# Optimization experiments

Hardware: AMD Instinct MI355X
Metric: run time of the kernel (lower is better)

## Reference

```python
import jax, jax.numpy as jnp
import numpy as np

B, C, DD, HH, WW = 1, 128, 16, 16, 16
D_STATE, D_CONV, EXPAND = 16, 4, 2
D_INNER = EXPAND * C
DT_RANK = (C + 15) // 16


def setup_inputs():
    key = jax.random.key(0)
    ks = jax.random.split(key, 10)
    def w(k, shape, s=0.02):
        return jax.random.normal(k, shape, dtype=jnp.float32) * s
    return {
        "x": jax.random.normal(ks[0], (B, C, DD, HH, WW), dtype=jnp.float32),
        "ln_w": jnp.ones((C,), jnp.float32),
        "ln_b": jnp.zeros((C,), jnp.float32),
        "mnorm_w": jnp.ones((C,), jnp.float32),
        "mnorm_b": jnp.zeros((C,), jnp.float32),
        "in_proj_w": w(ks[1], (2 * D_INNER, C)),
        "conv_w": w(ks[2], (D_INNER, D_CONV), 0.2),
        "conv_b": jnp.zeros((D_INNER,), jnp.float32),
        "x_proj_w": w(ks[3], (DT_RANK + 2 * D_STATE, D_INNER)),
        "dt_proj_w": w(ks[4], (D_INNER, DT_RANK), 0.1),
        "dt_proj_b": jnp.full((D_INNER,), float(np.log(np.expm1(0.01))), jnp.float32),
        "A_log": jnp.log(jnp.tile(jnp.arange(1, D_STATE + 1, dtype=jnp.float32), (D_INNER, 1))),
        "D_param": jnp.ones((D_INNER,), jnp.float32),
        "out_proj_w": w(ks[5], (C, D_INNER)),
        "proj_w": w(ks[6], (C, 3 * C)),
        "proj_b": jnp.zeros((C,), jnp.float32),
        "fc1_w": w(ks[7], (4 * C, C)),
        "fc1_b": jnp.zeros((4 * C,), jnp.float32),
        "fc2_w": w(ks[8], (C, 4 * C)),
        "fc2_b": jnp.zeros((C,), jnp.float32),
    }


def _ln_cf(x, w, b, eps=1e-6):
    # channels_first LayerNorm over axis 1 (matches custom LayerNorm)
    u = x.mean(1, keepdims=True)
    s = ((x - u) ** 2).mean(1, keepdims=True)
    xn = (x - u) * jax.lax.rsqrt(s + eps)
    return w[None, :, None, None, None] * xn + b[None, :, None, None, None]


def _ln_last(x, w, b, eps=1e-5):
    u = x.mean(-1, keepdims=True)
    s = ((x - u) ** 2).mean(-1, keepdims=True)
    return (x - u) * jax.lax.rsqrt(s + eps) * w + b


def _selective_scan(u, delta, A, Bm, Cm, Dv):
    # u, delta: (N,L,d); Bm,Cm: (N,L,n); A: (d,n); Dv: (d,)
    dA = jnp.exp(delta[..., None] * A)                               # (N,L,d,n)
    dBu = delta[..., None] * Bm[:, :, None, :] * u[..., None]         # (N,L,d,n)
    def step(h, inp):
        dA_t, dBu_t, C_t = inp
        h = dA_t * h + dBu_t
        y = jnp.einsum("bdn,bn->bd", h, C_t)
        return h, y
    h0 = jnp.zeros((u.shape[0], A.shape[0], A.shape[1]), u.dtype)
    _, ys = jax.lax.scan(step, h0, (dA.swapaxes(0, 1), dBu.swapaxes(0, 1), Cm.swapaxes(0, 1)))
    return ys.swapaxes(0, 1) + u * Dv


def _mamba(xin, in_proj_w, conv_w, conv_b, x_proj_w, dt_proj_w, dt_proj_b, A_log, D_param, out_proj_w):
    # xin: (N, L, C)
    N, L, _ = xin.shape
    xz = xin @ in_proj_w.T                                            # (N,L,2*d_inner)
    xr, z = jnp.split(xz, 2, axis=-1)
    # causal depthwise conv1d, kernel D_CONV, left-padded (mamba conv1d[..., :L])
    xp = jnp.pad(xr, ((0, 0), (D_CONV - 1, 0), (0, 0)))
    xc = sum(conv_w[:, k] * xp[:, k:k + L, :] for k in range(D_CONV)) + conv_b
    xc = jax.nn.silu(xc)
    x_dbl = xc @ x_proj_w.T                                           # (N,L,dt_rank+2n)
    dt = x_dbl[..., :DT_RANK]
    Bm = x_dbl[..., DT_RANK:DT_RANK + D_STATE]
    Cm = x_dbl[..., DT_RANK + D_STATE:]
    delta = jax.nn.softplus(dt @ dt_proj_w.T + dt_proj_b)
    A = -jnp.exp(A_log)
    y = _selective_scan(xc, delta, A, Bm, Cm, D_param)
    y = y * jax.nn.silu(z)
    return y @ out_proj_w.T


def _forward(x, ln_w, ln_b, mnorm_w, mnorm_b, in_proj_w, conv_w, conv_b, x_proj_w, dt_proj_w, dt_proj_b, A_log, D_param, out_proj_w, proj_w, proj_b, fc1_w, fc1_b, fc2_w, fc2_b):
    Bb, Cc, Dd, Hh, Ww = x.shape
    L = Dd * Hh * Ww
    x1 = _ln_cf(x, ln_w, ln_b)
    # three directional flattenings (d-, h-, w-major); cube => shapes identical
    xd = x1.reshape(Bb, Cc, L)
    xh = x1.transpose(0, 1, 3, 4, 2).reshape(Bb, Cc, L)
    xw = x1.transpose(0, 1, 4, 2, 3).reshape(Bb, Cc, L)
    seq = jnp.stack([xd, xh, xw], 0).reshape(3 * Bb, Cc, L).swapaxes(1, 2)  # (3B,L,C)
    seq = _ln_last(seq, mnorm_w, mnorm_b)
    y = _mamba(seq, in_proj_w, conv_w, conv_b, x_proj_w, dt_proj_w, dt_proj_b, A_log, D_param, out_proj_w)
    # reassemble per-direction volumes (no inverse permute, matching torch code) and concat on channels
    cat = y.swapaxes(1, 2).reshape(3, Bb, Cc, Dd, Hh, Ww).transpose(1, 0, 2, 3, 4, 5).reshape(Bb, 3 * Cc, Dd, Hh, Ww)
    out1 = jnp.einsum("bkdhw,ok->bodhw", cat, proj_w) + proj_b[None, :, None, None, None]
    out_res = x + out1
    h = _ln_cf(out_res, ln_w, ln_b)
    h = jnp.einsum("bcdhw,oc->bodhw", h, fc1_w) + fc1_b[None, :, None, None, None]
    h = jax.nn.gelu(h, approximate=False)
    h = jnp.einsum("bcdhw,oc->bodhw", h, fc2_w) + fc2_b[None, :, None, None, None]
    return h + out_res


def reference(x, ln_w, ln_b, mnorm_w, mnorm_b, in_proj_w, conv_w, conv_b, x_proj_w, dt_proj_w, dt_proj_b, A_log, D_param, out_proj_w, proj_w, proj_b, fc1_w, fc1_b, fc2_w, fc2_b):
    return _forward(x, ln_w, ln_b, mnorm_w, mnorm_b, in_proj_w, conv_w, conv_b, x_proj_w, dt_proj_w, dt_proj_b, A_log, D_param, out_proj_w, proj_w, proj_b, fc1_w, fc1_b, fc2_w, fc2_b)
```

## Files before the change

### kernel.cpp

```cpp
#include <hip/hip_runtime.h>
#include <hip/hip_bf16.h>
#include <math.h>

#define L 4096
#define C 128
#define DI 256
#define NST 16
#define NS 3
#define NCH 256
#define CT 16
#define R3 12288

typedef unsigned short u16;

__device__ __forceinline__ float siluf(float x){ return x / (1.f + __expf(-x)); }
__device__ __forceinline__ float geluf(float x){ return 0.5f*x*(1.f + erff(x*0.70710678118654752f)); }

__device__ __forceinline__ float b2f(u16 h){ return __uint_as_float(((unsigned)h)<<16); }
__device__ __forceinline__ u16 f2b(float f){
  unsigned u = __float_as_uint(f);
  return (u16)((u + 0x7FFFu + ((u>>16)&1u)) >> 16);
}
__device__ __forceinline__ float4 b4f(const u16* p){
  ushort4 v = *(const ushort4*)p;
  return make_float4(b2f(v.x), b2f(v.y), b2f(v.z), b2f(v.w));
}

__device__ __forceinline__ int permf(int s, int l){
  if(s==0) return l;
  if(s==1) return ((l&15)<<8) | ((l>>8)<<4) | ((l>>4)&15);
  return (((l>>4)&15)<<8) | ((l&15)<<4) | (l>>8);
}

__global__ void k_M(const float* __restrict__ opw, const float* __restrict__ pw,
                    float* __restrict__ Mw){
  int b = blockIdx.x;
  int o = b & 127, s = b >> 7;
  int d = threadIdx.x;
  float acc = 0.f;
  for(int c=0;c<C;c++) acc += opw[c*DI + d] * pw[o*384 + s*128 + c];
  Mw[(s*256+d)*128 + o] = acc;
}

__global__ void k_lngemm(const float* __restrict__ x, const float* __restrict__ lw,
                         const float* __restrict__ lb, const float* __restrict__ mw,
                         const float* __restrict__ mb, const float* __restrict__ ipw,
                         u16* __restrict__ Zb){
  __shared__ float As[128][68];
  __shared__ float Bs[64][132];
  int p0 = blockIdx.x*64, j0 = blockIdx.y*64;
  int tid = threadIdx.x;
  for(int q=0;q<8;q++){
    int f = q*1024 + tid*4; int cc = f>>6, p = f&63;
    float4 v = *(const float4*)&x[cc*L + p0 + p];
    *(float4*)&As[cc][p] = v;
  }
  for(int q=0;q<8;q++){
    int f = q*1024 + tid*4; int j = f>>7, k = f&127;
    float4 b = *(const float4*)&ipw[(j0+j)*C + k];
    *(float4*)&Bs[j][k] = b;
  }
  __syncthreads();
  {
    int p = tid>>2, kg = tid&3;
    float s=0.f, sq=0.f;
    #pragma unroll
    for(int i=0;i<32;i++){
      int k = kg*32 + ((i + kg*2)&31);
      float v = As[k][p]; s += v; sq += v*v;
    }
    s  += __shfl_xor(s,1);  s  += __shfl_xor(s,2);
    sq += __shfl_xor(sq,1); sq += __shfl_xor(sq,2);
    float m1 = s*(1.f/C);
    float r1 = rsqrtf(sq*(1.f/C) - m1*m1 + 1e-6f);
    float s2=0.f, sq2=0.f;
    #pragma unroll
    for(int i=0;i<32;i++){
      int k = kg*32 + ((i + kg*2)&31);
      float t = lw[k]*((As[k][p]-m1)*r1) + lb[k];
      s2 += t; sq2 += t*t;
    }
    s2  += __shfl_xor(s2,1);  s2  += __shfl_xor(s2,2);
    sq2 += __shfl_xor(sq2,1); sq2 += __shfl_xor(sq2,2);
    float m2 = s2*(1.f/C);
    float r2 = rsqrtf(sq2*(1.f/C) - m2*m2 + 1e-5f);
    #pragma unroll
    for(int i=0;i<32;i++){
      int k = kg*32 + ((i + kg*2)&31);
      float t = lw[k]*((As[k][p]-m1)*r1) + lb[k];
      As[k][p] = mw[k]*((t-m2)*r2) + mb[k];
    }
  }
  __syncthreads();
  int og = tid & 15, r4 = tid >> 4;
  float acc[4][4] = {};
  for(int k=0;k<128;k++){
    float4 av = *(const float4*)&As[k][r4*4];
    float a[4] = {av.x, av.y, av.z, av.w};
    float b[4];
    #pragma unroll
    for(int j=0;j<4;j++) b[j] = Bs[og+16*j][k];
    #pragma unroll
    for(int i=0;i<4;i++)
      #pragma unroll
      for(int j=0;j<4;j++) acc[i][j] += a[i]*b[j];
  }
  #pragma unroll
  for(int i=0;i<4;i++)
    #pragma unroll
    for(int j=0;j<4;j++)
      Zb[(p0+r4*4+i)*512 + j0 + og + 16*j] = f2b(acc[i][j]);
}

__global__ void k_conv(const u16* __restrict__ Zb, const float* __restrict__ cw,
                       const float* __restrict__ cb, u16* __restrict__ xcb){
  int bl = blockIdx.x;
  int s = bl >> 12, l = bl & 4095;
  int d = threadIdx.x;
  float acc = cb[d];
  #pragma unroll
  for(int k=0;k<4;k++){
    int lk = l - 3 + k;
    if(lk >= 0){
      int p = permf(s, lk);
      acc += cw[d*4+k] * b2f(Zb[p*512 + d]);
    }
  }
  xcb[bl*DI + d] = f2b(siluf(acc));
}

__global__ void k_xd4a(const u16* __restrict__ xcb, const float* __restrict__ xpw,
                       float* __restrict__ xp){
  __shared__ float As[32][132];
  __shared__ float Ws[40][132];
  int r0 = blockIdx.x*32;
  int k0 = blockIdx.y*128;
  int tid = threadIdx.x;
  for(int q=0;q<4;q++){
    int f = q*256 + tid; int r = f>>5, kk = (f&31)*4;
    float4 v = b4f(&xcb[(r0+r)*DI + k0 + kk]);
    *(float4*)&As[r][kk] = v;
  }
  for(int q=0;q<5;q++){
    int f = q*256 + tid; int col = f>>5, kk = (f&31)*4;
    float4 v = *(const float4*)&xpw[col*DI + k0 + kk];
    *(float4*)&Ws[col][kk] = v;
  }
  __syncthreads();
  int r = tid & 31, cg = tid >> 5;
  float acc[5] = {0.f,0.f,0.f,0.f,0.f};
  for(int k4=0;k4<32;k4++){
    float4 a = *(const float4*)&As[r][k4*4];
    #pragma unroll
    for(int j=0;j<5;j++){
      float4 w = *(const float4*)&Ws[cg*5+j][k4*4];
      acc[j] += a.x*w.x + a.y*w.y + a.z*w.z + a.w*w.w;
    }
  }
  float* dst = xp + (blockIdx.y*12288 + r0 + r)*40 + cg*5;
  #pragma unroll
  for(int j=0;j<5;j++) dst[j] = acc[j];
}

__global__ void k_xd4b(const float* __restrict__ xp, const float* __restrict__ dtw,
                       const float* __restrict__ dtb, float* __restrict__ Bc,
                       float* __restrict__ Cc, u16* __restrict__ deltab){
  __shared__ float xdb[40][17];
  int r0 = blockIdx.x*16;
  int tid = threadIdx.x;
  for(int e=tid; e<640; e+=256){
    int row = e/40, col = e%40;
    int idx = (r0+row)*40 + col;
    xdb[col][row] = xp[idx] + xp[491520 + idx];
  }
  __syncthreads();
  {
    float4 ww0 = *(const float4*)&dtw[tid*8];
    float4 ww1 = *(const float4*)&dtw[tid*8+4];
    float bb = dtb[tid];
    #pragma unroll 4
    for(int r=0;r<16;r++){
      float aa = bb + xdb[0][r]*ww0.x + xdb[1][r]*ww0.y + xdb[2][r]*ww0.z + xdb[3][r]*ww0.w
                    + xdb[4][r]*ww1.x + xdb[5][r]*ww1.y + xdb[6][r]*ww1.z + xdb[7][r]*ww1.w;
      float dl = (aa > 20.f) ? aa : log1pf(__expf(aa));
      deltab[(r0+r)*DI + tid] = f2b(dl);
    }
  }
  if(tid < 64){
    int rr = tid>>2, ng = (tid&3)*4;
    float4 bv = make_float4(xdb[8+ng][rr], xdb[9+ng][rr], xdb[10+ng][rr], xdb[11+ng][rr]);
    *(float4*)&Bc[(r0+rr)*NST + ng] = bv;
  } else if(tid < 128){
    int t2 = tid - 64;
    int rr = t2>>2, ng = (t2&3)*4;
    float4 cv = make_float4(xdb[24+ng][rr], xdb[25+ng][rr], xdb[26+ng][rr], xdb[27+ng][rr]);
    *(float4*)&Cc[(r0+rr)*NST + ng] = cv;
  }
}

__global__ void k_scanA(const u16* __restrict__ deltab, const u16* __restrict__ xcb,
                        const float* __restrict__ Bc, const float* __restrict__ A_log,
                        u16* __restrict__ aggAb, u16* __restrict__ aggBb){
  int b = blockIdx.x;
  int ng = b & 3, ch = (b>>2)&255, s = b>>10;
  int d = threadIdx.x;
  int n0 = ng*4;
  float Aa[4], P[4] = {1.f,1.f,1.f,1.f}, S[4] = {0.f,0.f,0.f,0.f};
  #pragma unroll
  for(int j=0;j<4;j++) Aa[j] = -__expf(A_log[d*NST + n0 + j]);
  int base = s*L + ch*CT;
  #pragma unroll
  for(int st=0; st<CT; st++){
    int row = base + st;
    float dl = b2f(deltab[row*DI + d]);
    float u  = b2f(xcb[row*DI + d]);
    float4 bv = *(const float4*)&Bc[row*NST + n0];
    float dlu = dl*u;
    float a;
    a = __expf(dl*Aa[0]); S[0] = a*S[0] + dlu*bv.x; P[0] *= a;
    a = __expf(dl*Aa[1]); S[1] = a*S[1] + dlu*bv.y; P[1] *= a;
    a = __expf(dl*Aa[2]); S[2] = a*S[2] + dlu*bv.z; P[2] *= a;
    a = __expf(dl*Aa[3]); S[3] = a*S[3] + dlu*bv.w; P[3] *= a;
  }
  int idx0 = ch*R3 + s*256 + d;
  #pragma unroll
  for(int j=0;j<4;j++){
    int idx = idx0 + (n0+j)*768;
    aggAb[idx] = f2b(P[j]); aggBb[idx] = f2b(S[j]);
  }
}

__global__ void k_scanB(const u16* __restrict__ aggAb, const u16* __restrict__ aggBb,
                        u16* __restrict__ hInb){
  __shared__ float PA[32][9], PB[32][9];
  int tid = threadIdx.x;
  int jl = tid & 31, seg = tid >> 5;
  int j = blockIdx.x*32 + jl;
  int c0 = seg*32;
  float pa[32], pb[32];
  float P = 1.f, S = 0.f;
  #pragma unroll
  for(int i=0;i<32;i++){
    pa[i] = P; pb[i] = S;
    float a = b2f(aggAb[(c0+i)*R3 + j]), b = b2f(aggBb[(c0+i)*R3 + j]);
    S = a*S + b; P = a*P;
  }
  PA[jl][seg] = P; PB[jl][seg] = S;
  __syncthreads();
  if(tid < 32){
    float h = 0.f;
    #pragma unroll
    for(int sg=0; sg<8; sg++){
      float p = PA[tid][sg], s2 = PB[tid][sg];
      PA[tid][sg] = h;
      h = p*h + s2;
    }
  }
  __syncthreads();
  float h0 = PA[jl][seg];
  #pragma unroll
  for(int i=0;i<32;i++){
    hInb[(c0+i)*R3 + j] = f2b(pa[i]*h0 + pb[i]);
  }
}

__global__ void k_scanC(const u16* __restrict__ deltab, const u16* __restrict__ xcb,
                        const float* __restrict__ Bc, const float* __restrict__ Cc,
                        const float* __restrict__ A_log, const float* __restrict__ Dp,
                        const u16* __restrict__ Zb, const u16* __restrict__ hInb,
                        u16* __restrict__ yzb){
  int b = blockIdx.x;
  int ch = b & 255, s = b >> 8;
  int d = threadIdx.x;
  float Aa[16], h[16];
  #pragma unroll
  for(int n=0;n<16;n++) Aa[n] = -__expf(A_log[d*NST + n]);
  #pragma unroll
  for(int n=0;n<16;n++) h[n] = b2f(hInb[ch*R3 + n*768 + s*256 + d]);
  float Dv = Dp[d];
  int base = s*L + ch*CT;
  #pragma unroll 2
  for(int st=0; st<CT; st++){
    int row = base + st;
    float dl = b2f(deltab[row*DI + d]);
    float u  = b2f(xcb[row*DI + d]);
    float dlu = dl*u;
    const float4* Bp = (const float4*)&Bc[row*NST];
    const float4* Cp = (const float4*)&Cc[row*NST];
    float y = u*Dv;
    #pragma unroll
    for(int q=0;q<4;q++){
      float4 bv = Bp[q], cv = Cp[q];
      float a;
      a = __expf(dl*Aa[4*q+0]); h[4*q+0] = a*h[4*q+0] + dlu*bv.x; y += h[4*q+0]*cv.x;
      a = __expf(dl*Aa[4*q+1]); h[4*q+1] = a*h[4*q+1] + dlu*bv.y; y += h[4*q+1]*cv.y;
      a = __expf(dl*Aa[4*q+2]); h[4*q+2] = a*h[4*q+2] + dlu*bv.z; y += h[4*q+2]*cv.z;
      a = __expf(dl*Aa[4*q+3]); h[4*q+3] = a*h[4*q+3] + dlu*bv.w; y += h[4*q+3]*cv.w;
    }
    int l = ch*CT + st;
    int p = permf(s, l);
    float zv = b2f(Zb[p*512 + 256 + d]);
    yzb[(s*L + l)*DI + d] = f2b(y * siluf(zv));
  }
}

__global__ void k_proj(const u16* __restrict__ yzb, const float* __restrict__ Mw,
                       u16* __restrict__ ppb){
  __shared__ float As[64][68];
  __shared__ float Bs[64][132];
  int p0 = blockIdx.x*64; int kc = blockIdx.y;
  int s = kc >> 1, d0 = (kc & 1)*128;
  int tid = threadIdx.x;
  int og = tid & 15, r4 = tid >> 4;
  float acc[4][8] = {};
  for(int kk=0; kk<2; kk++){
    int kb = d0 + kk*64;
    for(int q=0;q<4;q++){
      int f = q*256 + tid; int r = f>>4, k = (f&15)*4;
      float4 a = b4f(&yzb[(s*L + p0 + r)*DI + kb + k]);
      *(float4*)&As[r][k] = a;
    }
    for(int q=0;q<8;q++){
      int f = q*1024 + tid*4; int k = f>>7, o = f&127;
      float4 b = *(const float4*)&Mw[(s*256 + kb + k)*128 + o];
      *(float4*)&Bs[k][o] = b;
    }
    __syncthreads();
    for(int k=0;k<64;k++){
      float a[4];
      #pragma unroll
      for(int i=0;i<4;i++) a[i] = As[r4*4+i][k];
      #pragma unroll
      for(int j=0;j<8;j++){
        float bb = Bs[k][og+16*j];
        #pragma unroll
        for(int i=0;i<4;i++) acc[i][j] += a[i]*bb;
      }
    }
    __syncthreads();
  }
  u16* dst = ppb + kc*524288;
  #pragma unroll
  for(int i=0;i<4;i++)
    #pragma unroll
    for(int j=0;j<8;j++)
      dst[(p0+r4*4+i)*C + og + 16*j] = f2b(acc[i][j]);
}

__global__ void k_pred(const u16* __restrict__ ppb, const float* __restrict__ x,
                       const float* __restrict__ pb, float* __restrict__ ores){
  __shared__ float Xs[16][129];
  int p0 = blockIdx.x*16; int tid = threadIdx.x;
  for(int q=0;q<8;q++){
    int f = q*256 + tid; int pl = f&15, o = f>>4;
    Xs[pl][o] = x[o*L + p0 + pl];
  }
  __syncthreads();
  for(int q=0;q<8;q++){
    int f = q*256 + tid; int o = f&127, pl = f>>7;
    int idx = (p0+pl)*C + o;
    float v = b2f(ppb[idx]) + b2f(ppb[524288+idx]) + b2f(ppb[1048576+idx])
            + b2f(ppb[1572864+idx]) + b2f(ppb[2097152+idx]) + b2f(ppb[2621440+idx]);
    ores[idx] = v + Xs[pl][o] + pb[o];
  }
}

__global__ void k_fc1(const float* __restrict__ ores, const float* __restrict__ lw,
                      const float* __restrict__ lb, const float* __restrict__ w1,
                      const float* __restrict__ b1, u16* __restrict__ Hb){
  __shared__ float As[64][129];
  __shared__ float Bs[64][129];
  int p0 = blockIdx.x*64, j0 = blockIdx.y*64;
  int tid = threadIdx.x;
  for(int q=0;q<8;q++){
    int f = q*1024 + tid*4; int r = f>>7, k = f&127;
    float4 a = *(const float4*)&ores[(p0+r)*C + k];
    As[r][k]=a.x; As[r][k+1]=a.y; As[r][k+2]=a.z; As[r][k+3]=a.w;
    float4 b = *(const float4*)&w1[(j0+r)*C + k];
    Bs[r][k]=b.x; Bs[r][k+1]=b.y; Bs[r][k+2]=b.z; Bs[r][k+3]=b.w;
  }
  __syncthreads();
  {
    int r = tid>>2, kg = tid&3;
    float s=0.f, sq=0.f;
    #pragma unroll
    for(int i=0;i<32;i++){
      int k = kg*32 + ((i + kg*8)&31);
      float v = As[r][k]; s += v; sq += v*v;
    }
    s  += __shfl_xor(s,1);  s  += __shfl_xor(s,2);
    sq += __shfl_xor(sq,1); sq += __shfl_xor(sq,2);
    float m1 = s*(1.f/C);
    float r1 = rsqrtf(sq*(1.f/C) - m1*m1 + 1e-6f);
    #pragma unroll
    for(int i=0;i<32;i++){
      int k = kg*32 + ((i + kg*8)&31);
      As[r][k] = lw[k]*((As[r][k]-m1)*r1) + lb[k];
    }
  }
  __syncthreads();
  int og = tid & 15, r4 = tid >> 4;
  float acc[4][4] = {};
  for(int k=0;k<128;k++){
    float a[4], b[4];
    #pragma unroll
    for(int i=0;i<4;i++) a[i] = As[r4*4+i][k];
    #pragma unroll
    for(int j=0;j<4;j++) b[j] = Bs[og+16*j][k];
    #pragma unroll
    for(int i=0;i<4;i++)
      #pragma unroll
      for(int j=0;j<4;j++) acc[i][j] += a[i]*b[j];
  }
  #pragma unroll
  for(int i=0;i<4;i++)
    #pragma unroll
    for(int j=0;j<4;j++){
      int jj = j0 + og + 16*j;
      Hb[(p0+r4*4+i)*512 + jj] = f2b(geluf(acc[i][j] + b1[jj]));
    }
}

__global__ void k_fc2(const u16* __restrict__ Hb, const float* __restrict__ w2,
                      u16* __restrict__ fpb){
  __shared__ float As[64][68];
  __shared__ float Bs[128][68];
  int p0 = blockIdx.x*64; int kc = blockIdx.y;
  int tid = threadIdx.x;
  int og = tid & 15, r4 = tid >> 4;
  float acc[4][8] = {};
  for(int kk=0; kk<2; kk++){
    int kb = kc*128 + kk*64;
    for(int q=0;q<4;q++){
      int f = q*256 + tid; int r = f>>4, k = (f&15)*4;
      float4 a = b4f(&Hb[(p0+r)*512 + kb + k]);
      *(float4*)&As[r][k] = a;
    }
    for(int q=0;q<8;q++){
      int f = q*1024 + tid*4; int o = f>>6, k = f&63;
      float4 b = *(const float4*)&w2[o*512 + kb + k];
      *(float4*)&Bs[o][k] = b;
    }
    __syncthreads();
    for(int k=0;k<64;k++){
      float a[4];
      #pragma unroll
      for(int i=0;i<4;i++) a[i] = As[r4*4+i][k];
      #pragma unroll
      for(int j=0;j<8;j++){
        float bb = Bs[og+16*j][k];
        #pragma unroll
        for(int i=0;i<4;i++) acc[i][j] += a[i]*bb;
      }
    }
    __syncthreads();
  }
  u16* dst = fpb + kc*524288;
  #pragma unroll
  for(int i=0;i<4;i++)
    #pragma unroll
    for(int j=0;j<8;j++)
      dst[(p0+r4*4+i)*C + og + 16*j] = f2b(acc[i][j]);
}

__global__ void k_fred(const u16* __restrict__ fpb, const float* __restrict__ b2,
                       const float* __restrict__ ores, float* __restrict__ out){
  __shared__ float S[128][17];
  int p0 = blockIdx.x*16; int tid = threadIdx.x;
  for(int q=0;q<8;q++){
    int f = q*256 + tid; int o = f&127, pl = f>>7;
    int idx = (p0+pl)*C + o;
    float v = b2f(fpb[idx]) + b2f(fpb[524288+idx]) + b2f(fpb[1048576+idx]) + b2f(fpb[1572864+idx]);
    S[o][pl] = v + b2[o] + ores[idx];
  }
  __syncthreads();
  for(int q=0;q<8;q++){
    int f = q*256 + tid; int pl = f&15, o = f>>4;
    out[o*L + p0 + pl] = S[o][pl];
  }
}

extern "C" void kernel_launch(void* const* d_in, const int* in_sizes, int n_in,
                              void* d_out, int out_size, void* d_ws, size_t ws_size,
                              hipStream_t stream) {
  const float* x     = (const float*)d_in[0];
  const float* ln_w  = (const float*)d_in[1];
  const float* ln_b  = (const float*)d_in[2];
  const float* mw    = (const float*)d_in[3];
  const float* mb    = (const float*)d_in[4];
  const float* ipw   = (const float*)d_in[5];
  const float* cw    = (const float*)d_in[6];
  const float* cb    = (const float*)d_in[7];
  const float* xpw   = (const float*)d_in[8];
  const float* dtw   = (const float*)d_in[9];
  const float* dtb   = (const float*)d_in[10];
  const float* A_log = (const float*)d_in[11];
  const float* Dp    = (const float*)d_in[12];
  const float* opw   = (const float*)d_in[13];
  const float* pw    = (const float*)d_in[14];
  const float* pb    = (const float*)d_in[15];
  const float* w1    = (const float*)d_in[16];
  const float* b1    = (const float*)d_in[17];
  const float* w2    = (const float*)d_in[18];
  const float* b2    = (const float*)d_in[19];
  float* out = (float*)d_out;

  char* wsb = (char*)d_ws;
  u16* Zb     = (u16*)(wsb);
  u16* xcb    = (u16*)(wsb +  4194304);
  u16* deltab = (u16*)(wsb + 10485760);
  u16* aggAb  = (u16*)(wsb + 16777216);
  u16* aggBb  = (u16*)(wsb + 23068672);
  u16* hInb   = (u16*)(wsb + 29360128);
  float* Bc   = (float*)(wsb + 35651584);
  float* Cc   = (float*)(wsb + 36438016);
  float* Mw   = (float*)(wsb + 37224448);
  float* ores = (float*)(wsb + 37617664);
  float* xp   = (float*)(wsb + 39714816);
  u16* yzb = aggAb;
  u16* ppb = deltab;
  u16* Hb  = Zb;
  u16* fpb = xcb;

  k_M     <<<384, 256, 0, stream>>>(opw, pw, Mw);
  k_lngemm<<<dim3(64,8), 256, 0, stream>>>(x, ln_w, ln_b, mw, mb, ipw, Zb);
  k_conv  <<<NS*L, 256, 0, stream>>>(Zb, cw, cb, xcb);
  k_xd4a  <<<dim3(384,2), 256, 0, stream>>>(xcb, xpw, xp);
  k_xd4b  <<<768, 256, 0, stream>>>(xp, dtw, dtb, Bc, Cc, deltab);
  k_scanA <<<3072, 256, 0, stream>>>(deltab, xcb, Bc, A_log, aggAb, aggBb);
  k_scanB <<<384, 256, 0, stream>>>(aggAb, aggBb, hInb);
  k_scanC <<<768, 256, 0, stream>>>(deltab, xcb, Bc, Cc, A_log, Dp, Zb, hInb, yzb);
  k_proj  <<<dim3(64,6), 256, 0, stream>>>(yzb, Mw, ppb);
  k_pred  <<<256, 256, 0, stream>>>(ppb, x, pb, ores);
  k_fc1   <<<dim3(64,8), 256, 0, stream>>>(ores, ln_w, ln_b, w1, b1, Hb);
  k_fc2   <<<dim3(64,4), 256, 0, stream>>>(Hb, w2, fpb);
  k_fred  <<<256, 256, 0, stream>>>(fpb, b2, ores, out);
}
```

Before: 255.6 us.

## Merge front-end kernels and fuse x_proj with dt projection

Folds the weight-product precompute into the LN+in_proj GEMM launch as extra blocks, rewrites the depthwise conv so each thread slides a window over 16 positions for two channels, and fuses the split-K x_proj GEMM with the dt/B/C epilogue so the fp32 partials no longer round-trip through global memory. Five launches become three, with fewer launch gaps and less intermediate traffic. The price is that the fused x_proj kernel runs only 384 blocks doing the full K loop serially, which reduces parallelism, and the conv kernel has fewer, longer threads.

```diff
diff --git a/kernel.cpp b/kernel.cpp
--- a/kernel.cpp
+++ b/kernel.cpp
@@ -25,6 +25,13 @@
   ushort4 v = *(const ushort4*)p;
   return make_float4(b2f(v.x), b2f(v.y), b2f(v.z), b2f(v.w));
 }
+__device__ __forceinline__ float2 b2f2(const u16* p){
+  ushort2 v = *(const ushort2*)p;
+  return make_float2(b2f(v.x), b2f(v.y));
+}
+__device__ __forceinline__ ushort2 f2b2(float a, float b){
+  ushort2 r; r.x = f2b(a); r.y = f2b(b); return r;
+}
 
 __device__ __forceinline__ int permf(int s, int l){
   if(s==0) return l;
@@ -32,24 +39,24 @@
   return (((l>>4)&15)<<8) | ((l&15)<<4) | (l>>8);
 }
 
-__global__ void k_M(const float* __restrict__ opw, const float* __restrict__ pw,
-                    float* __restrict__ Mw){
-  int b = blockIdx.x;
-  int o = b & 127, s = b >> 7;
-  int d = threadIdx.x;
-  float acc = 0.f;
-  for(int c=0;c<C;c++) acc += opw[c*DI + d] * pw[o*384 + s*128 + c];
-  Mw[(s*256+d)*128 + o] = acc;
-}
-
-__global__ void k_lngemm(const float* __restrict__ x, const float* __restrict__ lw,
-                         const float* __restrict__ lb, const float* __restrict__ mw,
-                         const float* __restrict__ mb, const float* __restrict__ ipw,
-                         u16* __restrict__ Zb){
+__global__ void k_front(const float* __restrict__ x, const float* __restrict__ lw,
+                        const float* __restrict__ lb, const float* __restrict__ mw,
+                        const float* __restrict__ mb, const float* __restrict__ ipw,
+                        const float* __restrict__ opw, const float* __restrict__ pw,
+                        u16* __restrict__ Zb, float* __restrict__ Mw){
   __shared__ float As[128][68];
   __shared__ float Bs[64][132];
-  int p0 = blockIdx.x*64, j0 = blockIdx.y*64;
+  int bid = blockIdx.x;
   int tid = threadIdx.x;
+  if(bid < 384){
+    int o = bid & 127, s = bid >> 7;
+    float acc = 0.f;
+    for(int c=0;c<C;c++) acc += opw[c*DI + tid] * pw[o*384 + s*128 + c];
+    Mw[(s*256+tid)*128 + o] = acc;
+    return;
+  }
+  int b2 = bid - 384;
+  int p0 = (b2 & 63)*64, j0 = (b2 >> 6)*64;
   for(int q=0;q<8;q++){
     int f = q*1024 + tid*4; int cc = f>>6, p = f&63;
     float4 v = *(const float4*)&x[cc*L + p0 + p];
@@ -112,88 +119,89 @@
       Zb[(p0+r4*4+i)*512 + j0 + og + 16*j] = f2b(acc[i][j]);
 }
 
-__global__ void k_conv(const u16* __restrict__ Zb, const float* __restrict__ cw,
-                       const float* __restrict__ cb, u16* __restrict__ xcb){
+__global__ void k_conv2(const u16* __restrict__ Zb, const float* __restrict__ cw,
+                        const float* __restrict__ cb, u16* __restrict__ xcb){
   int bl = blockIdx.x;
-  int s = bl >> 12, l = bl & 4095;
-  int d = threadIdx.x;
-  float acc = cb[d];
-  #pragma unroll
-  for(int k=0;k<4;k++){
-    int lk = l - 3 + k;
-    if(lk >= 0){
-      int p = permf(s, lk);
-      acc += cw[d*4+k] * b2f(Zb[p*512 + d]);
-    }
-  }
-  xcb[bl*DI + d] = f2b(siluf(acc));
-}
-
-__global__ void k_xd4a(const u16* __restrict__ xcb, const float* __restrict__ xpw,
-                       float* __restrict__ xp){
+  int s = bl >> 8, l0 = (bl & 255)*16;
+  int t = threadIdx.x;
+  int d0 = t*2;
+  float w00=cw[d0*4+0], w01=cw[d0*4+1], w02=cw[d0*4+2], w03=cw[d0*4+3];
+  float w10=cw[d0*4+4], w11=cw[d0*4+5], w12=cw[d0*4+6], w13=cw[d0*4+7];
+  float bb0=cb[d0], bb1=cb[d0+1];
+  float2 h0 = make_float2(0.f,0.f), h1 = h0, h2 = h0;
+  if(l0 > 0){
+    h0 = b2f2(&Zb[permf(s,l0-3)*512 + d0]);
+    h1 = b2f2(&Zb[permf(s,l0-2)*512 + d0]);
+    h2 = b2f2(&Zb[permf(s,l0-1)*512 + d0]);
+  }
+  #pragma unroll 4
+  for(int st=0; st<16; st++){
+    int l = l0 + st;
+    float2 cur = b2f2(&Zb[permf(s,l)*512 + d0]);
+    float o0 = bb0 + w00*h0.x + w01*h1.x + w02*h2.x + w03*cur.x;
+    float o1 = bb1 + w10*h0.y + w11*h1.y + w12*h2.y + w13*cur.y;
+    *(ushort2*)&xcb[(s*L + l)*DI + d0] = f2b2(siluf(o0), siluf(o1));
+    h0 = h1; h1 = h2; h2 = cur;
+  }
+}
+
+__global__ void k_xd5(const u16* __restrict__ xcb, const float* __restrict__ xpw,
+                      const float* __restrict__ dtw, const float* __restrict__ dtb,
+                      float* __restrict__ Bc, float* __restrict__ Cc,
+                      u16* __restrict__ deltab){
   __shared__ float As[32][132];
   __shared__ float Ws[40][132];
+  __shared__ float BCs[40][33];
   int r0 = blockIdx.x*32;
-  int k0 = blockIdx.y*128;
   int tid = threadIdx.x;
-  for(int q=0;q<4;q++){
-    int f = q*256 + tid; int r = f>>5, kk = (f&31)*4;
-    float4 v = b4f(&xcb[(r0+r)*DI + k0 + kk]);
-    *(float4*)&As[r][kk] = v;
-  }
-  for(int q=0;q<5;q++){
-    int f = q*256 + tid; int col = f>>5, kk = (f&31)*4;
-    float4 v = *(const float4*)&xpw[col*DI + k0 + kk];
-    *(float4*)&Ws[col][kk] = v;
-  }
-  __syncthreads();
   int r = tid & 31, cg = tid >> 5;
   float acc[5] = {0.f,0.f,0.f,0.f,0.f};
-  for(int k4=0;k4<32;k4++){
-    float4 a = *(const float4*)&As[r][k4*4];
-    #pragma unroll
-    for(int j=0;j<5;j++){
-      float4 w = *(const float4*)&Ws[cg*5+j][k4*4];
-      acc[j] += a.x*w.x + a.y*w.y + a.z*w.z + a.w*w.w;
-    }
-  }
-  float* dst = xp + (blockIdx.y*12288 + r0 + r)*40 + cg*5;
-  #pragma unroll
-  for(int j=0;j<5;j++) dst[j] = acc[j];
-}
-
-__global__ void k_xd4b(const float* __restrict__ xp, const float* __restrict__ dtw,
-                       const float* __restrict__ dtb, float* __restrict__ Bc,
-                       float* __restrict__ Cc, u16* __restrict__ deltab){
-  __shared__ float xdb[40][17];
-  int r0 = blockIdx.x*16;
-  int tid = threadIdx.x;
-  for(int e=tid; e<640; e+=256){
-    int row = e/40, col = e%40;
-    int idx = (r0+row)*40 + col;
-    xdb[col][row] = xp[idx] + xp[491520 + idx];
-  }
+  for(int ph=0; ph<2; ph++){
+    int k0 = ph*128;
+    for(int q=0;q<4;q++){
+      int f = q*256 + tid; int rr = f>>5, kk = (f&31)*4;
+      float4 v = b4f(&xcb[(r0+rr)*DI + k0 + kk]);
+      *(float4*)&As[rr][kk] = v;
+    }
+    for(int q=0;q<5;q++){
+      int f = q*256 + tid; int col = f>>5, kk = (f&31)*4;
+      float4 v = *(const float4*)&xpw[col*DI + k0 + kk];
+      *(float4*)&Ws[col][kk] = v;
+    }
+    __syncthreads();
+    for(int k4=0;k4<32;k4++){
+      float4 a = *(const float4*)&As[r][k4*4];
+      #pragma unroll
+      for(int j=0;j<5;j++){
+        float4 w = *(const float4*)&Ws[cg*5+j][k4*4];
+        acc[j] += a.x*w.x + a.y*w.y + a.z*w.z + a.w*w.w;
+      }
+    }
+    __syncthreads();
+  }
+  #pragma unroll
+  for(int j=0;j<5;j++) BCs[cg*5+j][r] = acc[j];
   __syncthreads();
   {
     float4 ww0 = *(const float4*)&dtw[tid*8];
     float4 ww1 = *(const float4*)&dtw[tid*8+4];
     float bb = dtb[tid];
     #pragma unroll 4
-    for(int r=0;r<16;r++){
-      float aa = bb + xdb[0][r]*ww0.x + xdb[1][r]*ww0.y + xdb[2][r]*ww0.z + xdb[3][r]*ww0.w
-                    + xdb[4][r]*ww1.x + xdb[5][r]*ww1.y + xdb[6][r]*ww1.z + xdb[7][r]*ww1.w;
+    for(int rr=0;rr<32;rr++){
+      float aa = bb + BCs[0][rr]*ww0.x + BCs[1][rr]*ww0.y + BCs[2][rr]*ww0.z + BCs[3][rr]*ww0.w
+                    + BCs[4][rr]*ww1.x + BCs[5][rr]*ww1.y + BCs[6][rr]*ww1.z + BCs[7][rr]*ww1.w;
       float dl = (aa > 20.f) ? aa : log1pf(__expf(aa));
-      deltab[(r0+r)*DI + tid] = f2b(dl);
-    }
-  }
-  if(tid < 64){
+      deltab[(r0+rr)*DI + tid] = f2b(dl);
+    }
+  }
+  if(tid < 128){
     int rr = tid>>2, ng = (tid&3)*4;
-    float4 bv = make_float4(xdb[8+ng][rr], xdb[9+ng][rr], xdb[10+ng][rr], xdb[11+ng][rr]);
+    float4 bv = make_float4(BCs[ 8+ng][rr], BCs[ 9+ng][rr], BCs[10+ng][rr], BCs[11+ng][rr]);
     *(float4*)&Bc[(r0+rr)*NST + ng] = bv;
-  } else if(tid < 128){
-    int t2 = tid - 64;
+  } else {
+    int t2 = tid - 128;
     int rr = t2>>2, ng = (t2&3)*4;
-    float4 cv = make_float4(xdb[24+ng][rr], xdb[25+ng][rr], xdb[26+ng][rr], xdb[27+ng][rr]);
+    float4 cv = make_float4(BCs[24+ng][rr], BCs[25+ng][rr], BCs[26+ng][rr], BCs[27+ng][rr]);
     *(float4*)&Cc[(r0+rr)*NST + ng] = cv;
   }
 }
@@ -516,17 +524,14 @@
   float* Cc   = (float*)(wsb + 36438016);
   float* Mw   = (float*)(wsb + 37224448);
   float* ores = (float*)(wsb + 37617664);
-  float* xp   = (float*)(wsb + 39714816);
   u16* yzb = aggAb;
   u16* ppb = deltab;
   u16* Hb  = Zb;
   u16* fpb = xcb;
 
-  k_M     <<<384, 256, 0, stream>>>(opw, pw, Mw);
-  k_lngemm<<<dim3(64,8), 256, 0, stream>>>(x, ln_w, ln_b, mw, mb, ipw, Zb);
-  k_conv  <<<NS*L, 256, 0, stream>>>(Zb, cw, cb, xcb);
-  k_xd4a  <<<dim3(384,2), 256, 0, stream>>>(xcb, xpw, xp);
-  k_xd4b  <<<768, 256, 0, stream>>>(xp, dtw, dtb, Bc, Cc, deltab);
+  k_front <<<896, 256, 0, stream>>>(x, ln_w, ln_b, mw, mb, ipw, opw, pw, Zb, Mw);
+  k_conv2 <<<768, 128, 0, stream>>>(Zb, cw, cb, xcb);
+  k_xd5   <<<384, 256, 0, stream>>>(xcb, xpw, dtw, dtb, Bc, Cc, deltab);
   k_scanA <<<3072, 256, 0, stream>>>(deltab, xcb, Bc, A_log, aggAb, aggBb);
   k_scanB <<<384, 256, 0, stream>>>(aggAb, aggBb, hInb);
   k_scanC <<<768, 256, 0, stream>>>(deltab, xcb, Bc, Cc, A_log, Dp, Zb, hInb, yzb);
```

New measurement: 260.2 us. Within noise of the previous version (+1.8%).
